# Optimization experiments

Hardware: AMD Instinct MI355X
Metric: run time of the kernel (lower is better)

The kernel has to match this reference:

```python
import jax, jax.numpy as jnp
import numpy as np

N = 32768       # total nodes = NUM_GRAPHS * T
F_IN = 32       # num_features
HC = 64         # hidden_channels
HEADS = 4
E = 524288      # edges before self-loops
NUM_GRAPHS = 64 # == batch.max()+1 by construction
T = 512         # time steps per graph (N // NUM_GRAPHS)
OUT = 24        # output_size
NEG_SLOPE = 0.2 # PyG GATConv default


def gat_layer(x, src, dst, W, a_src, a_dst, b, n_nodes):
    """PyG GATConv (concat=True) with edge softmax over incoming edges."""
    H, C = a_src.shape
    h = (x @ W).reshape(n_nodes, H, C)                    # [N,H,C]
    alpha_src = jnp.sum(h * a_src, axis=-1)               # [N,H]
    alpha_dst = jnp.sum(h * a_dst, axis=-1)               # [N,H]
    e = jax.nn.leaky_relu(alpha_src[src] + alpha_dst[dst], NEG_SLOPE)  # [E,H]
    m = jax.ops.segment_max(e, dst, num_segments=n_nodes)
    e = jnp.exp(e - m[dst])
    s = jax.ops.segment_sum(e, dst, num_segments=n_nodes)
    alpha = e / (s[dst] + 1e-16)                          # [E,H]
    msg = h[src] * alpha[..., None]                       # [E,H,C]
    out = jax.ops.segment_sum(msg, dst, num_segments=n_nodes)  # [N,H,C]
    return out.reshape(n_nodes, H * C) + b


def gru_layer(x, Wih, Whh, bih, bhh):
    """torch nn.GRU single layer, batch_first input x: [B,T,Hin] -> ([B,T,H], h_T)."""
    Bsz = x.shape[0]
    H = Whh.shape[1]

    def step(h, xt):
        gi = xt @ Wih.T + bih
        gh = h @ Whh.T + bhh
        ir, iz, inn = jnp.split(gi, 3, axis=-1)
        hr, hz, hn = jnp.split(gh, 3, axis=-1)
        r = jax.nn.sigmoid(ir + hr)
        z = jax.nn.sigmoid(iz + hz)
        n = jnp.tanh(inn + r * hn)
        h_new = (1.0 - z) * n + z * h
        return h_new, h_new

    h0 = jnp.zeros((Bsz, H), x.dtype)
    hT, ys = jax.lax.scan(step, h0, jnp.swapaxes(x, 0, 1))
    return jnp.swapaxes(ys, 0, 1), hT


def setup_inputs() -> dict:
    key = jax.random.key(0)
    ks = jax.random.split(key, 24)
    sc = 0.1
    inp = {
        "x": jax.random.normal(ks[0], (N, F_IN), dtype=jnp.float32),
        "edge_index": jax.random.randint(ks[1], (2, E), 0, N, dtype=jnp.int32),
        "batch": jnp.repeat(jnp.arange(NUM_GRAPHS, dtype=jnp.int32), T),
        # GAT layer 1: F_IN -> HC x HEADS (concat)
        "W1": sc * jax.random.normal(ks[2], (F_IN, HEADS * HC), dtype=jnp.float32),
        "a_src1": sc * jax.random.normal(ks[3], (HEADS, HC), dtype=jnp.float32),
        "a_dst1": sc * jax.random.normal(ks[4], (HEADS, HC), dtype=jnp.float32),
        "b1": jnp.zeros((HEADS * HC,), dtype=jnp.float32),
        # GAT layer 2: HEADS*HC -> HC, 1 head
        "W2": sc * jax.random.normal(ks[5], (HEADS * HC, HC), dtype=jnp.float32),
        "a_src2": sc * jax.random.normal(ks[6], (1, HC), dtype=jnp.float32),
        "a_dst2": sc * jax.random.normal(ks[7], (1, HC), dtype=jnp.float32),
        "b2": jnp.zeros((HC,), dtype=jnp.float32),
        # GRU (2 layers, input_size == hidden_size == HC)
        "gru_Wih0": sc * jax.random.normal(ks[8], (3 * HC, HC), dtype=jnp.float32),
        "gru_Whh0": sc * jax.random.normal(ks[9], (3 * HC, HC), dtype=jnp.float32),
        "gru_bih0": jnp.zeros((3 * HC,), dtype=jnp.float32),
        "gru_bhh0": jnp.zeros((3 * HC,), dtype=jnp.float32),
        "gru_Wih1": sc * jax.random.normal(ks[10], (3 * HC, HC), dtype=jnp.float32),
        "gru_Whh1": sc * jax.random.normal(ks[11], (3 * HC, HC), dtype=jnp.float32),
        "gru_bih1": jnp.zeros((3 * HC,), dtype=jnp.float32),
        "gru_bhh1": jnp.zeros((3 * HC,), dtype=jnp.float32),
        # Linear head
        "Wl": sc * jax.random.normal(ks[12], (OUT, HC), dtype=jnp.float32),
        "bl": jnp.zeros((OUT,), dtype=jnp.float32),
    }
    return inp


def reference(x, edge_index, batch, W1, a_src1, a_dst1, b1, W2, a_src2, a_dst2, b2,
              gru_Wih0, gru_Whh0, gru_bih0, gru_bhh0,
              gru_Wih1, gru_Whh1, gru_bih1, gru_bhh1, Wl, bl):
    # PyG GATConv default add_self_loops=True
    loops = jnp.arange(N, dtype=edge_index.dtype)
    src = jnp.concatenate([edge_index[0], loops])
    dst = jnp.concatenate([edge_index[1], loops])

    h = jax.nn.elu(gat_layer(x, src, dst, W1, a_src1, a_dst1, b1, N))   # [N, HEADS*HC]
    h = jax.nn.elu(gat_layer(h, src, dst, W2, a_src2, a_dst2, b2, N))   # [N, HC]

    # batch is repeat(arange(NUM_GRAPHS), T) so batch.max()+1 == NUM_GRAPHS (static)
    seq = h.reshape(NUM_GRAPHS, T, HC)
    seq, _ = gru_layer(seq, gru_Wih0, gru_Whh0, gru_bih0, gru_bhh0)
    _, hT = gru_layer(seq, gru_Wih1, gru_Whh1, gru_bih1, gru_bhh1)      # [B, HC]
    return hT @ Wl.T + bl                                               # [B, OUT]
```

## Files before the change

### kernel.cpp

```cpp
#include <hip/hip_runtime.h>
#include <hip/hip_bf16.h>

#define N_NODES 32768
#define F_IN    32
#define HC      64
#define HEADS   4
#define NE      524288
#define NET     (NE + N_NODES)
#define NG      64
#define TT      512
#define OUTF    24

__device__ __forceinline__ float lrelu(float x){ return x > 0.f ? x : 0.2f*x; }
__device__ __forceinline__ float eluf (float x){ return x > 0.f ? x : __expf(x)-1.f; }
__device__ __forceinline__ float sigmf(float x){ return 1.f/(1.f+__expf(-x)); }
__device__ __forceinline__ float tanhfast(float x){ return 1.f - 2.f/(__expf(2.f*x)+1.f); }
__device__ __forceinline__ float bcast(float v, int k){
  return __int_as_float(__builtin_amdgcn_readlane(__float_as_int(v), k));
}

__global__ __launch_bounds__(256) void k_deg(const int* __restrict__ ei,
                                             int* __restrict__ deg){
  int e = blockIdx.x*256 + threadIdx.x;
  int d = (e < NE) ? ei[NE+e] : (e - NE);
  atomicAdd(deg + d, 1);
}

__global__ __launch_bounds__(1024) void k_scan(const int* __restrict__ deg,
                                               int* __restrict__ rowptr){
  __shared__ int ps[1024];
  const int t = threadIdx.x;
  const int base = t*32;
  int local[32]; int s = 0;
  #pragma unroll
  for(int i=0;i<32;i++){ local[i]=deg[base+i]; s+=local[i]; }
  ps[t]=s; __syncthreads();
  for(int off=1; off<1024; off<<=1){
    int v = (t>=off) ? ps[t-off] : 0;
    __syncthreads();
    ps[t]+=v;
    __syncthreads();
  }
  int run = (t==0) ? 0 : ps[t-1];
  #pragma unroll
  for(int i=0;i<32;i++){ rowptr[base+i]=run; run+=local[i]; }
  if(t==1023) rowptr[N_NODES]=run;
}

__global__ __launch_bounds__(256) void k_fill(const int* __restrict__ ei,
                                              const int* __restrict__ rowptr,
                                              int* __restrict__ cur,
                                              int* __restrict__ col){
  int e = blockIdx.x*256 + threadIdx.x;
  int s, d;
  if(e < NE){ s = ei[e]; d = ei[NE+e]; } else { s = e-NE; d = s; }
  int pos = atomicAdd(cur + d, 1);
  col[rowptr[d] + pos] = s;
}

__global__ __launch_bounds__(256) void k_alpha1x(const float* __restrict__ x,
                                                 const float* __restrict__ W1,
                                                 const float* __restrict__ a_src,
                                                 const float* __restrict__ a_dst,
                                                 float* __restrict__ as1,
                                                 float* __restrict__ ad1){
  __shared__ float ps[256];
  const int tid = threadIdx.x;
  {
    const int k = tid>>3, q = tid&7;
    const int h = q>>1, isd = q&1;
    const float* av = (isd ? a_dst : a_src) + h*64;
    const float* wr = W1 + k*256 + h*64;
    float acc = 0.f;
    #pragma unroll
    for(int c=0;c<64;c++) acc += wr[c]*av[c];
    ps[(isd?128:0) + k*4 + h] = acc;
  }
  __syncthreads();
  const int n = blockIdx.x*256 + tid;
  const float4* xr = (const float4*)(x + n*32);
  float sa0=0.f,sa1=0.f,sa2=0.f,sa3=0.f, sd0=0.f,sd1=0.f,sd2=0.f,sd3=0.f;
  #pragma unroll
  for(int k4=0;k4<8;k4++){
    float4 v = xr[k4];
    const float* pa = ps + (4*k4)*4;
    const float* pd = ps + 128 + (4*k4)*4;
    sa0 += v.x*pa[0] + v.y*pa[4] + v.z*pa[8]  + v.w*pa[12];
    sa1 += v.x*pa[1] + v.y*pa[5] + v.z*pa[9]  + v.w*pa[13];
    sa2 += v.x*pa[2] + v.y*pa[6] + v.z*pa[10] + v.w*pa[14];
    sa3 += v.x*pa[3] + v.y*pa[7] + v.z*pa[11] + v.w*pa[15];
    sd0 += v.x*pd[0] + v.y*pd[4] + v.z*pd[8]  + v.w*pd[12];
    sd1 += v.x*pd[1] + v.y*pd[5] + v.z*pd[9]  + v.w*pd[13];
    sd2 += v.x*pd[2] + v.y*pd[6] + v.z*pd[10] + v.w*pd[14];
    sd3 += v.x*pd[3] + v.y*pd[7] + v.z*pd[11] + v.w*pd[15];
  }
  *(float4*)(as1+n*4) = make_float4(sa0,sa1,sa2,sa3);
  *(float4*)(ad1+n*4) = make_float4(sd0,sd1,sd2,sd3);
}

__global__ __launch_bounds__(256) void k_gatx(const int* __restrict__ rowptr,
                                              const int* __restrict__ col,
                                              const float* __restrict__ as1,
                                              const float* __restrict__ ad1,
                                              const float* __restrict__ x,
                                              float* __restrict__ agg,
                                              float* __restrict__ s14){
  const int node = blockIdx.x*4 + (threadIdx.x>>6);
  const int lane = threadIdx.x & 63;
  const int h0   = lane>>5;
  const int c    = lane & 31;
  const int beg = rowptr[node], end = rowptr[node+1];
  const float adA = ad1[node*4 + h0];
  const float adB = ad1[node*4 + h0 + 2];
  float accA=0.f, accB=0.f, wsA=0.f, wsB=0.f;
  int j = beg;
  for(; j+3 < end; j += 4){
    int s0 = col[j], s1 = col[j+1], s2 = col[j+2], s3 = col[j+3];
    float4 q0 = *(const float4*)(as1 + s0*4);
    float4 q1 = *(const float4*)(as1 + s1*4);
    float4 q2 = *(const float4*)(as1 + s2*4);
    float4 q3 = *(const float4*)(as1 + s3*4);
    float x0 = x[s0*32 + c];
    float x1 = x[s1*32 + c];
    float x2 = x[s2*32 + c];
    float x3 = x[s3*32 + c];
    float wA0 = __expf(lrelu((h0?q0.y:q0.x) + adA));
    float wA1 = __expf(lrelu((h0?q1.y:q1.x) + adA));
    float wA2 = __expf(lrelu((h0?q2.y:q2.x) + adA));
    float wA3 = __expf(lrelu((h0?q3.y:q3.x) + adA));
    float wB0 = __expf(lrelu((h0?q0.w:q0.z) + adB));
    float wB1 = __expf(lrelu((h0?q1.w:q1.z) + adB));
    float wB2 = __expf(lrelu((h0?q2.w:q2.z) + adB));
    float wB3 = __expf(lrelu((h0?q3.w:q3.z) + adB));
    accA += wA0*x0 + wA1*x1 + wA2*x2 + wA3*x3;
    accB += wB0*x0 + wB1*x1 + wB2*x2 + wB3*x3;
    wsA  += (wA0+wA1) + (wA2+wA3);
    wsB  += (wB0+wB1) + (wB2+wB3);
  }
  for(; j < end; j++){
    int s0 = col[j];
    float4 q0 = *(const float4*)(as1 + s0*4);
    float wA0 = __expf(lrelu((h0?q0.y:q0.x) + adA));
    float wB0 = __expf(lrelu((h0?q0.w:q0.z) + adB));
    float x0 = x[s0*32 + c];
    accA += wA0*x0; accB += wB0*x0;
    wsA += wA0; wsB += wB0;
  }
  agg[node*128 + h0*32 + c]     = accA;
  agg[node*128 + (h0+2)*32 + c] = accB;
  if(c == 0){
    s14[node*4 + h0]     = wsA;
    s14[node*4 + h0 + 2] = wsB;
  }
}

__global__ __launch_bounds__(256) void k_g12(const float* __restrict__ agg,
                                             const float* __restrict__ W1,
                                             const float* __restrict__ s14,
                                             const float* __restrict__ b1,
                                             const float* __restrict__ W2,
                                             const float* __restrict__ a_src2,
                                             const float* __restrict__ a_dst2,
                                             float* __restrict__ h2,
                                             float* __restrict__ as2,
                                             float* __restrict__ ad2){
  __shared__ __align__(16) float ags[32*128];
  __shared__ __align__(16) float o1s[32*256];
  __shared__ float sv[128];
  const int tid  = threadIdx.x;
  const int row0 = blockIdx.x*32;
  const float4* ag = (const float4*)(agg + (size_t)row0*128);
  float4* a4 = (float4*)ags;
  for(int i=tid;i<1024;i+=256) a4[i]=ag[i];
  if(tid<32) ((float4*)sv)[tid]=((const float4*)(s14+row0*4))[tid];
  float wc[32];
  #pragma unroll
  for(int k=0;k<32;k++) wc[k]=W1[k*256+tid];
  const float bb=b1[tid];
  __syncthreads();
  const int h = tid>>6;
  for(int r=0;r<32;r++){
    const float4* ar=(const float4*)(ags + r*128 + h*32);
    float acc=0.f;
    #pragma unroll
    for(int k4=0;k4<8;k4++){
      float4 v=ar[k4];
      acc += v.x*wc[4*k4]+v.y*wc[4*k4+1]+v.z*wc[4*k4+2]+v.w*wc[4*k4+3];
    }
    float inv = 1.f/(sv[r*4+h] + 1e-16f);
    o1s[r*256+tid] = eluf(acc*inv + bb);
  }
  __syncthreads();
  const int c0=(tid&15)*4;
  const int r0=(tid>>4)*2;
  float acc2[2][4]={};
  for(int k=0;k<256;k+=4){
    float wv[4][4];
    #pragma unroll
    for(int i=0;i<4;i++){
      float4 w=*(const float4*)(W2+(k+i)*64+c0);
      wv[i][0]=w.x; wv[i][1]=w.y; wv[i][2]=w.z; wv[i][3]=w.w;
    }
    #pragma unroll
    for(int i=0;i<2;i++){
      float4 xv=*(const float4*)(o1s+(r0+i)*256+k);
      #pragma unroll
      for(int j=0;j<4;j++)
        acc2[i][j]+=xv.x*wv[0][j]+xv.y*wv[1][j]+xv.z*wv[2][j]+xv.w*wv[3][j];
    }
  }
  float* h2s = ags;
  #pragma unroll
  for(int i=0;i<2;i++){
    float4 o = make_float4(acc2[i][0],acc2[i][1],acc2[i][2],acc2[i][3]);
    *(float4*)(h2 + (size_t)(row0+r0+i)*64 + c0) = o;
    *(float4*)(h2s + (r0+i)*64 + c0) = o;
  }
  __syncthreads();
  if(tid < 32){
    const float4* hp=(const float4*)(h2s + tid*64);
    float sa=0.f, sd=0.f;
    #pragma unroll
    for(int i=0;i<16;i++){
      float4 v=hp[i];
      float4 a=((const float4*)a_src2)[i];
      float4 d=((const float4*)a_dst2)[i];
      sa+=v.x*a.x+v.y*a.y+v.z*a.z+v.w*a.w;
      sd+=v.x*d.x+v.y*d.y+v.z*d.z+v.w*d.w;
    }
    as2[row0+tid]=sa; ad2[row0+tid]=sd;
  }
}

__global__ __launch_bounds__(256) void k_gat2(const int* __restrict__ rowptr,
                                              const int* __restrict__ col,
                                              const float* __restrict__ as2,
                                              const float* __restrict__ ad2,
                                              const float* __restrict__ h2,
                                              const float* __restrict__ b2,
                                              float* __restrict__ out2){
  const int node = blockIdx.x*4 + (threadIdx.x>>6);
  const int lane = threadIdx.x & 63;
  const int beg = rowptr[node], end = rowptr[node+1];
  const float ad = ad2[node];
  float acc = 0.f, s = 0.f;
  int j = beg;
  for(; j+3 < end; j += 4){
    int s0 = col[j], s1 = col[j+1], s2 = col[j+2], s3 = col[j+3];
    float a0 = as2[s0], a1 = as2[s1], a2 = as2[s2], a3 = as2[s3];
    float v0 = h2[s0*64+lane], v1 = h2[s1*64+lane];
    float v2 = h2[s2*64+lane], v3 = h2[s3*64+lane];
    float w0 = __expf(lrelu(a0 + ad));
    float w1 = __expf(lrelu(a1 + ad));
    float w2 = __expf(lrelu(a2 + ad));
    float w3 = __expf(lrelu(a3 + ad));
    acc += w0*v0 + w1*v1 + w2*v2 + w3*v3;
    s += (w0+w1) + (w2+w3);
  }
  for(; j < end; j++){
    int s0 = col[j];
    float w0 = __expf(lrelu(as2[s0] + ad));
    acc += w0*h2[s0*64+lane];
    s += w0;
  }
  const float inv = 1.f/(s + 1e-16f);
  out2[node*64+lane] = eluf(acc*inv + b2[lane]);
}

__global__ __launch_bounds__(256) void k_gemm_gi(const float* __restrict__ in,
                                                 const float* __restrict__ Wih,
                                                 const float* __restrict__ bih,
                                                 float* __restrict__ gi){
  __shared__ __align__(16) float xs[64*64];
  __shared__ float wT[64*192];
  const int tid=threadIdx.x;
  const int row0=blockIdx.x*64;
  const float4* xg=(const float4*)(in+row0*64);
  float4* xs4=(float4*)xs;
  for(int i=tid;i<1024;i+=256) xs4[i]=xg[i];
  for(int i=tid;i<12288;i+=256){ wT[(i&63)*192+(i>>6)] = Wih[i]; }
  __syncthreads();
  if(tid<192){
    float wr[64];
    #pragma unroll
    for(int k=0;k<64;k++) wr[k]=wT[k*192+tid];
    const float bj=bih[tid];
    for(int r=0;r<64;r++){
      float acc=bj;
      const float4* xr=(const float4*)(xs+r*64);
      #pragma unroll
      for(int k4=0;k4<16;k4++){
        float4 v=xr[k4];
        acc+=v.x*wr[4*k4]+v.y*wr[4*k4+1]+v.z*wr[4*k4+2]+v.w*wr[4*k4+3];
      }
      gi[(row0+r)*192+tid]=acc;
    }
  }
}

__global__ __launch_bounds__(384,1) void k_gru6(const float* __restrict__ gi1,
                                                const float* __restrict__ Whh0,
                                                const float* __restrict__ bhh0,
                                                const float* __restrict__ Wih1,
                                                const float* __restrict__ bih1,
                                                const float* __restrict__ Whh1,
                                                const float* __restrict__ bhh1,
                                                const float* __restrict__ Wl,
                                                const float* __restrict__ bl,
                                                float* __restrict__ fout){
  __shared__ float h1s[64];
  __shared__ float h2s[64];
  __shared__ float gh1p[2][192];
  __shared__ float gi2p[2][192];
  __shared__ float gh2p[2][192];
  __shared__ float g1r[2][192];
  const int tid  = threadIdx.x;
  const int w    = tid >> 6;
  const int lane = tid & 63;
  const int kh   = (w >= 3) ? 1 : 0;
  const int m    = (w >= 3) ? (w-3) : w;
  const int b    = blockIdx.x;
  const float* gib = gi1 + (size_t)b*TT*192;

  const float* W  = (m==0) ? Whh0 : (m==1) ? Wih1 : Whh1;
  const float* bb = (m==0) ? bhh0 : (m==1) ? bih1 : bhh1;
  float* dst      = (m==0) ? gh1p[kh] : (m==1) ? gi2p[kh] : gh2p[kh];

  const int kof = kh*32;
  const float4* pa = (const float4*)(W + lane*64       + kof);
  const float4* pb = (const float4*)(W + (64+lane)*64  + kof);
  const float4* pc = (const float4*)(W + (128+lane)*64 + kof);
  float4 Av0=pa[0], Av1=pa[1], Av2=pa[2], Av3=pa[3];
  float4 Av4=pa[4], Av5=pa[5], Av6=pa[6], Av7=pa[7];
  float4 Bv0=pb[0], Bv1=pb[1], Bv2=pb[2], Bv3=pb[3];
  float4 Bv4=pb[4], Bv5=pb[5], Bv6=pb[6], Bv7=pb[7];
  float4 Cv0=pc[0], Cv1=pc[1], Cv2=pc[2], Cv3=pc[3];
  float4 Cv4=pc[4], Cv5=pc[5], Cv6=pc[6], Cv7=pc[7];
  const float biasA = kh ? 0.f : bb[lane];
  const float biasB = kh ? 0.f : bb[64+lane];
  const float biasC = kh ? 0.f : bb[128+lane];

  float giv = 0.f;
  if(w >= 3){
    const int c = (w-3)*64 + lane;
    g1r[0][c] = gib[c];
    giv = gib[192 + c];
  }
  if(tid < 64){ h1s[tid]=0.f; h2s[tid]=0.f; }
  __syncthreads();

  const float* hs = (m==2) ? h2s : h1s;
  const int hidx = (lane + kof) & 63;

  for(int i=0;i<=TT;i++){
    float hv = hs[hidx];
    if(w >= 3){
      const int c = (w-3)*64 + lane;
      int pst = i+1;
      if(pst < TT) g1r[pst&1][c] = giv;
      int nst = i+2;
      if(nst < TT) giv = gib[(size_t)nst*192 + c];
    }
    float a0=biasA, a1=0.f, a2=0.f, a3=0.f;
    float b0=biasB, b1_=0.f, b2_=0.f, b3=0.f;
    float c0=biasC, c1=0.f, c2=0.f, c3=0.f;
#define DOT4(WA, WB, WC, BASE) { \
    float t0=bcast(hv,BASE+0), t1=bcast(hv,BASE+1), t2=bcast(hv,BASE+2), t3=bcast(hv,BASE+3); \
    a0 = fmaf(t0, WA.x, a0);  b0  = fmaf(t0, WB.x, b0);  c0 = fmaf(t0, WC.x, c0); \
    a1 = fmaf(t1, WA.y, a1);  b1_ = fmaf(t1, WB.y, b1_); c1 = fmaf(t1, WC.y, c1); \
    a2 = fmaf(t2, WA.z, a2);  b2_ = fmaf(t2, WB.z, b2_); c2 = fmaf(t2, WC.z, c2); \
    a3 = fmaf(t3, WA.w, a3);  b3  = fmaf(t3, WB.w, b3);  c3 = fmaf(t3, WC.w, c3); }
    DOT4(Av0,Bv0,Cv0, 0)  DOT4(Av1,Bv1,Cv1, 4)  DOT4(Av2,Bv2,Cv2, 8)  DOT4(Av3,Bv3,Cv3, 12)
    DOT4(Av4,Bv4,Cv4, 16) DOT4(Av5,Bv5,Cv5, 20) DOT4(Av6,Bv6,Cv6, 24) DOT4(Av7,Bv7,Cv7, 28)
#undef DOT4
    dst[lane]     = (a0+a1)+(a2+a3);
    dst[64+lane]  = (b0+b1_)+(b2_+b3);
    dst[128+lane] = (c0+c1)+(c2+c3);
    __syncthreads();
    if(w == 0){
      if(i < TT){
        float G0 = gh1p[0][lane]      + gh1p[1][lane];
        float G1 = gh1p[0][64+lane]   + gh1p[1][64+lane];
        float G2 = gh1p[0][128+lane]  + gh1p[1][128+lane];
        float r = sigmf(g1r[i&1][lane]     + G0);
        float z = sigmf(g1r[i&1][64+lane]  + G1);
        float n = tanhfast(g1r[i&1][128+lane] + r*G2);
        h1s[lane] = (1.f-z)*n + z*h1s[lane];
      }
    } else if(w == 2){
      if(i >= 1){
        float I0 = gi2p[0][lane]      + gi2p[1][lane];
        float I1 = gi2p[0][64+lane]   + gi2p[1][64+lane];
        float I2 = gi2p[0][128+lane]  + gi2p[1][128+lane];
        float G0 = gh2p[0][lane]      + gh2p[1][lane];
        float G1 = gh2p[0][64+lane]   + gh2p[1][64+lane];
        float G2 = gh2p[0][128+lane]  + gh2p[1][128+lane];
        float r = sigmf(I0 + G0);
        float z = sigmf(I1 + G1);
        float n = tanhfast(I2 + r*G2);
        h2s[lane] = (1.f-z)*n + z*h2s[lane];
      }
    }
    __syncthreads();
  }

  if(tid < 24){
    float acc = bl[tid];
    const float4* wl4 = (const float4*)(Wl + tid*64);
    #pragma unroll
    for(int k4=0;k4<16;k4++){
      float4 h4 = *(const float4*)(h2s + 4*k4);
      float4 w4 = wl4[k4];
      acc += h4.x*w4.x + h4.y*w4.y + h4.z*w4.z + h4.w*w4.w;
    }
    fout[b*24+tid] = acc;
  }
}

extern "C" void kernel_launch(void* const* d_in, const int* in_sizes, int n_in,
                              void* d_out, int out_size, void* d_ws, size_t ws_size,
                              hipStream_t stream){
  const float* x     =(const float*)d_in[0];
  const int*   ei    =(const int*  )d_in[1];
  const float* W1    =(const float*)d_in[3];
  const float* a_src1=(const float*)d_in[4];
  const float* a_dst1=(const float*)d_in[5];
  const float* b1    =(const float*)d_in[6];
  const float* W2    =(const float*)d_in[7];
  const float* a_src2=(const float*)d_in[8];
  const float* a_dst2=(const float*)d_in[9];
  const float* b2    =(const float*)d_in[10];
  const float* Wih0  =(const float*)d_in[11];
  const float* Whh0  =(const float*)d_in[12];
  const float* bih0  =(const float*)d_in[13];
  const float* bhh0  =(const float*)d_in[14];
  const float* Wih1  =(const float*)d_in[15];
  const float* Whh1  =(const float*)d_in[16];
  const float* bih1  =(const float*)d_in[17];
  const float* bhh1  =(const float*)d_in[18];
  const float* Wl    =(const float*)d_in[19];
  const float* bl    =(const float*)d_in[20];

  float* ws   = (float*)d_ws;
  float* agg  = ws;
  float* s14  = ws + 4194304;
  float* gi   = ws;
  float* out2 = ws + 8388608;
  float* h2   = ws + 16777216;
  float* as1  = ws + 18874368;
  float* ad1  = as1 + 131072;
  float* as2  = ad1 + 131072;
  float* ad2  = as2 + 32768;
  int* rowptr = (int*)(ad2 + 32768);
  int* deg    = rowptr + 32800;
  int* cur    = deg + 32768;
  int* col    = cur + 32768;
  float* fo   = (float*)d_out;

  hipMemsetAsync(deg, 0, 2*32768*sizeof(int), stream);

  k_deg   <<<2176,256,0,stream>>>(ei,deg);
  k_scan  <<<1  ,1024,0,stream>>>(deg,rowptr);
  k_fill  <<<2176,256,0,stream>>>(ei,rowptr,cur,col);

  k_alpha1x<<<128 ,256,0,stream>>>(x,W1,a_src1,a_dst1,as1,ad1);
  k_gatx   <<<8192,256,0,stream>>>(rowptr,col,as1,ad1,x,agg,s14);
  k_g12    <<<1024,256,0,stream>>>(agg,W1,s14,b1,W2,a_src2,a_dst2,h2,as2,ad2);
  k_gat2   <<<8192,256,0,stream>>>(rowptr,col,as2,ad2,h2,b2,out2);
  k_gemm_gi<<<512 ,256,0,stream>>>(out2,Wih0,bih0,gi);
  k_gru6   <<<64  ,384,0,stream>>>(gi,Whh0,bhh0,Wih1,bih1,Whh1,bhh1,Wl,bl,fo);
  (void)in_sizes; (void)n_in; (void)out_size; (void)ws_size;
}
```

Before: 734.7 us.

## Split fused two-layer GRU into single-wave per-layer kernels with batched input GEMM

Replaces the 384-thread fused two-layer GRU kernel, which used shared memory and two barriers per step, with two 64-thread single-wavefront kernels. Each lane holds a full 64-wide weight row for all three gates in registers, so the recurrence needs no barriers or shared-memory partial sums. The layer-2 input projection is moved out of the recurrence into a separate parallel GEMM over the stored layer-1 sequence. This trades the two-layer wavefront pipelining for twice the serial step count, plus extra global traffic and register pressure (192 pinned weight VGPRs per lane).

```diff
diff --git a/kernel.cpp b/kernel.cpp
--- a/kernel.cpp
+++ b/kernel.cpp
@@ -17,6 +17,9 @@
 __device__ __forceinline__ float tanhfast(float x){ return 1.f - 2.f/(__expf(2.f*x)+1.f); }
 __device__ __forceinline__ float bcast(float v, int k){
   return __int_as_float(__builtin_amdgcn_readlane(__float_as_int(v), k));
+}
+__device__ __forceinline__ void pin4(float4 &v){
+  asm volatile("" : "+v"(v.x), "+v"(v.y), "+v"(v.z), "+v"(v.w));
 }
 
 __global__ __launch_bounds__(256) void k_deg(const int* __restrict__ ei,
@@ -298,122 +301,131 @@
   }
 }
 
-__global__ __launch_bounds__(384,1) void k_gru6(const float* __restrict__ gi1,
-                                                const float* __restrict__ Whh0,
-                                                const float* __restrict__ bhh0,
-                                                const float* __restrict__ Wih1,
-                                                const float* __restrict__ bih1,
-                                                const float* __restrict__ Whh1,
-                                                const float* __restrict__ bhh1,
-                                                const float* __restrict__ Wl,
-                                                const float* __restrict__ bl,
-                                                float* __restrict__ fout){
-  __shared__ float h1s[64];
-  __shared__ float h2s[64];
-  __shared__ float gh1p[2][192];
-  __shared__ float gi2p[2][192];
-  __shared__ float gh2p[2][192];
-  __shared__ float g1r[2][192];
-  const int tid  = threadIdx.x;
-  const int w    = tid >> 6;
-  const int lane = tid & 63;
-  const int kh   = (w >= 3) ? 1 : 0;
-  const int m    = (w >= 3) ? (w-3) : w;
+#define GRU_W_LOAD(W)                                             \
+  const float4* pa = (const float4*)((W) + lane*64);              \
+  const float4* pb = (const float4*)((W) + (64+lane)*64);         \
+  const float4* pc = (const float4*)((W) + (128+lane)*64);        \
+  float4 Av0=pa[0], Av1=pa[1], Av2=pa[2],  Av3=pa[3];             \
+  float4 Av4=pa[4], Av5=pa[5], Av6=pa[6],  Av7=pa[7];             \
+  float4 Av8=pa[8], Av9=pa[9], AvA=pa[10], AvB=pa[11];            \
+  float4 AvC=pa[12],AvD=pa[13],AvE=pa[14], AvF=pa[15];            \
+  float4 Bv0=pb[0], Bv1=pb[1], Bv2=pb[2],  Bv3=pb[3];             \
+  float4 Bv4=pb[4], Bv5=pb[5], Bv6=pb[6],  Bv7=pb[7];             \
+  float4 Bv8=pb[8], Bv9=pb[9], BvA=pb[10], BvB=pb[11];            \
+  float4 BvC=pb[12],BvD=pb[13],BvE=pb[14], BvF=pb[15];            \
+  float4 Cv0=pc[0], Cv1=pc[1], Cv2=pc[2],  Cv3=pc[3];             \
+  float4 Cv4=pc[4], Cv5=pc[5], Cv6=pc[6],  Cv7=pc[7];             \
+  float4 Cv8=pc[8], Cv9=pc[9], CvA=pc[10], CvB=pc[11];            \
+  float4 CvC=pc[12],CvD=pc[13],CvE=pc[14], CvF=pc[15];            \
+  pin4(Av0);pin4(Av1);pin4(Av2);pin4(Av3);pin4(Av4);pin4(Av5);    \
+  pin4(Av6);pin4(Av7);pin4(Av8);pin4(Av9);pin4(AvA);pin4(AvB);    \
+  pin4(AvC);pin4(AvD);pin4(AvE);pin4(AvF);                        \
+  pin4(Bv0);pin4(Bv1);pin4(Bv2);pin4(Bv3);pin4(Bv4);pin4(Bv5);    \
+  pin4(Bv6);pin4(Bv7);pin4(Bv8);pin4(Bv9);pin4(BvA);pin4(BvB);    \
+  pin4(BvC);pin4(BvD);pin4(BvE);pin4(BvF);                        \
+  pin4(Cv0);pin4(Cv1);pin4(Cv2);pin4(Cv3);pin4(Cv4);pin4(Cv5);    \
+  pin4(Cv6);pin4(Cv7);pin4(Cv8);pin4(Cv9);pin4(CvA);pin4(CvB);    \
+  pin4(CvC);pin4(CvD);pin4(CvE);pin4(CvF);
+
+#define DOT4S(WA, WB, WC, BASE) {                                                   \
+  float t0=bcast(hv,BASE+0), t1=bcast(hv,BASE+1), t2=bcast(hv,BASE+2), t3=bcast(hv,BASE+3); \
+  a0 = fmaf(t0, WA.x, a0);  b0 = fmaf(t0, WB.x, b0);  c0 = fmaf(t0, WC.x, c0);      \
+  a1 = fmaf(t1, WA.y, a1);  b1 = fmaf(t1, WB.y, b1);  c1 = fmaf(t1, WC.y, c1);      \
+  a2 = fmaf(t2, WA.z, a2);  b2 = fmaf(t2, WB.z, b2);  c2 = fmaf(t2, WC.z, c2);      \
+  a3 = fmaf(t3, WA.w, a3);  b3 = fmaf(t3, WB.w, b3);  c3 = fmaf(t3, WC.w, c3); }
+
+#define GRU_MATVEC()                                                  \
+  float a0=biasA, a1=0.f, a2=0.f, a3=0.f;                             \
+  float b0=biasB, b1=0.f, b2=0.f, b3=0.f;                             \
+  float c0=biasC, c1=0.f, c2=0.f, c3=0.f;                             \
+  float hv = h;                                                       \
+  DOT4S(Av0,Bv0,Cv0, 0)  DOT4S(Av1,Bv1,Cv1, 4)                        \
+  DOT4S(Av2,Bv2,Cv2, 8)  DOT4S(Av3,Bv3,Cv3, 12)                       \
+  DOT4S(Av4,Bv4,Cv4, 16) DOT4S(Av5,Bv5,Cv5, 20)                       \
+  DOT4S(Av6,Bv6,Cv6, 24) DOT4S(Av7,Bv7,Cv7, 28)                       \
+  DOT4S(Av8,Bv8,Cv8, 32) DOT4S(Av9,Bv9,Cv9, 36)                       \
+  DOT4S(AvA,BvA,CvA, 40) DOT4S(AvB,BvB,CvB, 44)                       \
+  DOT4S(AvC,BvC,CvC, 48) DOT4S(AvD,BvD,CvD, 52)                       \
+  DOT4S(AvE,BvE,CvE, 56) DOT4S(AvF,BvF,CvF, 60)                       \
+  float ghA=(a0+a1)+(a2+a3);                                          \
+  float ghB=(b0+b1)+(b2+b3);                                          \
+  float ghC=(c0+c1)+(c2+c3);
+
+__global__ __launch_bounds__(64,1) void k_gru_l1(const float* __restrict__ gi1,
+                                                 const float* __restrict__ Whh,
+                                                 const float* __restrict__ bhh,
+                                                 float* __restrict__ seq){
+  const int lane = threadIdx.x;
   const int b    = blockIdx.x;
   const float* gib = gi1 + (size_t)b*TT*192;
-
-  const float* W  = (m==0) ? Whh0 : (m==1) ? Wih1 : Whh1;
-  const float* bb = (m==0) ? bhh0 : (m==1) ? bih1 : bhh1;
-  float* dst      = (m==0) ? gh1p[kh] : (m==1) ? gi2p[kh] : gh2p[kh];
-
-  const int kof = kh*32;
-  const float4* pa = (const float4*)(W + lane*64       + kof);
-  const float4* pb = (const float4*)(W + (64+lane)*64  + kof);
-  const float4* pc = (const float4*)(W + (128+lane)*64 + kof);
-  float4 Av0=pa[0], Av1=pa[1], Av2=pa[2], Av3=pa[3];
-  float4 Av4=pa[4], Av5=pa[5], Av6=pa[6], Av7=pa[7];
-  float4 Bv0=pb[0], Bv1=pb[1], Bv2=pb[2], Bv3=pb[3];
-  float4 Bv4=pb[4], Bv5=pb[5], Bv6=pb[6], Bv7=pb[7];
-  float4 Cv0=pc[0], Cv1=pc[1], Cv2=pc[2], Cv3=pc[3];
-  float4 Cv4=pc[4], Cv5=pc[5], Cv6=pc[6], Cv7=pc[7];
-  const float biasA = kh ? 0.f : bb[lane];
-  const float biasB = kh ? 0.f : bb[64+lane];
-  const float biasC = kh ? 0.f : bb[128+lane];
-
-  float giv = 0.f;
-  if(w >= 3){
-    const int c = (w-3)*64 + lane;
-    g1r[0][c] = gib[c];
-    giv = gib[192 + c];
-  }
-  if(tid < 64){ h1s[tid]=0.f; h2s[tid]=0.f; }
-  __syncthreads();
-
-  const float* hs = (m==2) ? h2s : h1s;
-  const int hidx = (lane + kof) & 63;
-
-  for(int i=0;i<=TT;i++){
-    float hv = hs[hidx];
-    if(w >= 3){
-      const int c = (w-3)*64 + lane;
-      int pst = i+1;
-      if(pst < TT) g1r[pst&1][c] = giv;
-      int nst = i+2;
-      if(nst < TT) giv = gib[(size_t)nst*192 + c];
-    }
-    float a0=biasA, a1=0.f, a2=0.f, a3=0.f;
-    float b0=biasB, b1_=0.f, b2_=0.f, b3=0.f;
-    float c0=biasC, c1=0.f, c2=0.f, c3=0.f;
-#define DOT4(WA, WB, WC, BASE) { \
-    float t0=bcast(hv,BASE+0), t1=bcast(hv,BASE+1), t2=bcast(hv,BASE+2), t3=bcast(hv,BASE+3); \
-    a0 = fmaf(t0, WA.x, a0);  b0  = fmaf(t0, WB.x, b0);  c0 = fmaf(t0, WC.x, c0); \
-    a1 = fmaf(t1, WA.y, a1);  b1_ = fmaf(t1, WB.y, b1_); c1 = fmaf(t1, WC.y, c1); \
-    a2 = fmaf(t2, WA.z, a2);  b2_ = fmaf(t2, WB.z, b2_); c2 = fmaf(t2, WC.z, c2); \
-    a3 = fmaf(t3, WA.w, a3);  b3  = fmaf(t3, WB.w, b3);  c3 = fmaf(t3, WC.w, c3); }
-    DOT4(Av0,Bv0,Cv0, 0)  DOT4(Av1,Bv1,Cv1, 4)  DOT4(Av2,Bv2,Cv2, 8)  DOT4(Av3,Bv3,Cv3, 12)
-    DOT4(Av4,Bv4,Cv4, 16) DOT4(Av5,Bv5,Cv5, 20) DOT4(Av6,Bv6,Cv6, 24) DOT4(Av7,Bv7,Cv7, 28)
-#undef DOT4
-    dst[lane]     = (a0+a1)+(a2+a3);
-    dst[64+lane]  = (b0+b1_)+(b2_+b3);
-    dst[128+lane] = (c0+c1)+(c2+c3);
-    __syncthreads();
-    if(w == 0){
-      if(i < TT){
-        float G0 = gh1p[0][lane]      + gh1p[1][lane];
-        float G1 = gh1p[0][64+lane]   + gh1p[1][64+lane];
-        float G2 = gh1p[0][128+lane]  + gh1p[1][128+lane];
-        float r = sigmf(g1r[i&1][lane]     + G0);
-        float z = sigmf(g1r[i&1][64+lane]  + G1);
-        float n = tanhfast(g1r[i&1][128+lane] + r*G2);
-        h1s[lane] = (1.f-z)*n + z*h1s[lane];
-      }
-    } else if(w == 2){
-      if(i >= 1){
-        float I0 = gi2p[0][lane]      + gi2p[1][lane];
-        float I1 = gi2p[0][64+lane]   + gi2p[1][64+lane];
-        float I2 = gi2p[0][128+lane]  + gi2p[1][128+lane];
-        float G0 = gh2p[0][lane]      + gh2p[1][lane];
-        float G1 = gh2p[0][64+lane]   + gh2p[1][64+lane];
-        float G2 = gh2p[0][128+lane]  + gh2p[1][128+lane];
-        float r = sigmf(I0 + G0);
-        float z = sigmf(I1 + G1);
-        float n = tanhfast(I2 + r*G2);
-        h2s[lane] = (1.f-z)*n + z*h2s[lane];
-      }
-    }
-    __syncthreads();
-  }
-
-  if(tid < 24){
-    float acc = bl[tid];
-    const float4* wl4 = (const float4*)(Wl + tid*64);
+  GRU_W_LOAD(Whh)
+  const float biasA = bhh[lane];
+  const float biasB = bhh[64+lane];
+  const float biasC = bhh[128+lane];
+  float h = 0.f;
+  float gA = gib[lane],       gB = gib[64+lane],       gC = gib[128+lane];
+  float nA = gib[192+lane],   nB = gib[192+64+lane],   nC = gib[192+128+lane];
+  float* sq = seq + (size_t)b*TT*64 + lane;
+  for(int t=0;t<TT;t++){
+    float fA=0.f, fB=0.f, fC=0.f;
+    if(t+2 < TT){
+      const float* g2 = gib + (size_t)(t+2)*192;
+      fA = g2[lane]; fB = g2[64+lane]; fC = g2[128+lane];
+    }
+    GRU_MATVEC()
+    float r = sigmf(gA + ghA);
+    float z = sigmf(gB + ghB);
+    float n = tanhfast(gC + r*ghC);
+    h = (1.f-z)*n + z*h;
+    sq[(size_t)t*64] = h;
+    gA = nA; gB = nB; gC = nC;
+    nA = fA; nB = fB; nC = fC;
+  }
+}
+
+__global__ __launch_bounds__(64,1) void k_gru_l2(const float* __restrict__ gi2,
+                                                 const float* __restrict__ Whh,
+                                                 const float* __restrict__ bhh,
+                                                 const float* __restrict__ Wl,
+                                                 const float* __restrict__ bl,
+                                                 float* __restrict__ fout){
+  __shared__ float hf[64];
+  const int lane = threadIdx.x;
+  const int b    = blockIdx.x;
+  const float* gib = gi2 + (size_t)b*TT*192;
+  GRU_W_LOAD(Whh)
+  const float biasA = bhh[lane];
+  const float biasB = bhh[64+lane];
+  const float biasC = bhh[128+lane];
+  float h = 0.f;
+  float gA = gib[lane],       gB = gib[64+lane],       gC = gib[128+lane];
+  float nA = gib[192+lane],   nB = gib[192+64+lane],   nC = gib[192+128+lane];
+  for(int t=0;t<TT;t++){
+    float fA=0.f, fB=0.f, fC=0.f;
+    if(t+2 < TT){
+      const float* g2 = gib + (size_t)(t+2)*192;
+      fA = g2[lane]; fB = g2[64+lane]; fC = g2[128+lane];
+    }
+    GRU_MATVEC()
+    float r = sigmf(gA + ghA);
+    float z = sigmf(gB + ghB);
+    float n = tanhfast(gC + r*ghC);
+    h = (1.f-z)*n + z*h;
+    gA = nA; gB = nB; gC = nC;
+    nA = fA; nB = fB; nC = fC;
+  }
+  hf[lane] = h;
+  __syncthreads();
+  if(lane < 24){
+    float acc = bl[lane];
+    const float4* wl4 = (const float4*)(Wl + lane*64);
     #pragma unroll
     for(int k4=0;k4<16;k4++){
-      float4 h4 = *(const float4*)(h2s + 4*k4);
+      float4 h4 = *(const float4*)(hf + 4*k4);
       float4 w4 = wl4[k4];
       acc += h4.x*w4.x + h4.y*w4.y + h4.z*w4.z + h4.w*w4.w;
     }
-    fout[b*24+tid] = acc;
+    fout[b*24+lane] = acc;
   }
 }
 
@@ -444,8 +456,10 @@
   float* ws   = (float*)d_ws;
   float* agg  = ws;
   float* s14  = ws + 4194304;
-  float* gi   = ws;
+  float* gi1  = ws;
   float* out2 = ws + 8388608;
+  float* seq  = ws + 8388608;
+  float* gi2  = ws + 10485760;
   float* h2   = ws + 16777216;
   float* as1  = ws + 18874368;
   float* ad1  = as1 + 131072;
@@ -467,7 +481,9 @@
   k_gatx   <<<8192,256,0,stream>>>(rowptr,col,as1,ad1,x,agg,s14);
   k_g12    <<<1024,256,0,stream>>>(agg,W1,s14,b1,W2,a_src2,a_dst2,h2,as2,ad2);
   k_gat2   <<<8192,256,0,stream>>>(rowptr,col,as2,ad2,h2,b2,out2);
-  k_gemm_gi<<<512 ,256,0,stream>>>(out2,Wih0,bih0,gi);
-  k_gru6   <<<64  ,384,0,stream>>>(gi,Whh0,bhh0,Wih1,bih1,Whh1,bhh1,Wl,bl,fo);
+  k_gemm_gi<<<512 ,256,0,stream>>>(out2,Wih0,bih0,gi1);
+  k_gru_l1 <<<64  ,64 ,0,stream>>>(gi1,Whh0,bhh0,seq);
+  k_gemm_gi<<<512 ,256,0,stream>>>(seq,Wih1,bih1,gi2);
+  k_gru_l2 <<<64  ,64 ,0,stream>>>(gi2,Whh1,bhh1,Wl,bl,fo);
   (void)in_sizes; (void)n_in; (void)out_size; (void)ws_size;
 }
```

Result: slower. 944.9 us (+28.6%).
